# Kernel tuning notes

Hardware: AMD Instinct MI355X
Metric: run time of the kernel (lower is better)

Reference implementation:

```python
import jax, jax.numpy as jnp
import numpy as np

B, T, F = 32, 1024, 64
H = 128          # num_lstm_out
KH = 16          # kan_hidden_dim
C1, C2, C3 = 128, 256, 128
NC = 10


def _glorot(key, shape):
    fan_in = shape[0] if len(shape) == 2 else int(np.prod(shape[1:]))
    return (jax.random.normal(key, shape, jnp.float32) / np.sqrt(fan_in)).astype(jnp.float32)


def setup_inputs() -> dict:
    key = jax.random.key(0)
    ks = jax.random.split(key, 24)
    D = F + H
    d = {}
    d['x'] = jax.random.normal(ks[0], (B, T, F), jnp.float32)
    d['eps_z'] = jax.random.normal(ks[1], (B, H), jnp.float32)
    d['eps_cat'] = jax.random.normal(ks[2], (B, H), jnp.float32)
    # KAN-LSTM cell: gates = W2 @ silu(W1 @ [x;h])
    d['kan_w1'] = _glorot(ks[3], (D, KH)); d['kan_b1'] = jnp.zeros((KH,), jnp.float32)
    d['kan_w2'] = _glorot(ks[4], (KH, 4 * H)); d['kan_b2'] = jnp.zeros((4 * H,), jnp.float32)
    # causal convs (OIH layout)
    d['conv1_w'] = _glorot(ks[5], (C1, F, 8)); d['conv1_b'] = jnp.zeros((C1,), jnp.float32)
    d['conv2_w'] = _glorot(ks[6], (C2, C1, 5)); d['conv2_b'] = jnp.zeros((C2,), jnp.float32)
    d['conv3_w'] = _glorot(ks[7], (C3, C2, 3)); d['conv3_b'] = jnp.zeros((C3,), jnp.float32)
    # batchnorm affine params
    d['bn1_g'] = jnp.ones((C1,), jnp.float32); d['bn1_b'] = jnp.zeros((C1,), jnp.float32)
    d['bn2_g'] = jnp.ones((C2,), jnp.float32); d['bn2_b'] = jnp.zeros((C2,), jnp.float32)
    d['bn3_g'] = jnp.ones((C3,), jnp.float32); d['bn3_b'] = jnp.zeros((C3,), jnp.float32)
    # SE layers (reduction=16, no bias)
    d['se1_w1'] = _glorot(ks[8], (C1, C1 // 16)); d['se1_w2'] = _glorot(ks[9], (C1 // 16, C1))
    d['se2_w1'] = _glorot(ks[10], (C2, C2 // 16)); d['se2_w2'] = _glorot(ks[11], (C2 // 16, C2))
    # VIB heads
    d['fc_mu_w'] = _glorot(ks[12], (H, H)); d['fc_mu_b'] = jnp.zeros((H,), jnp.float32)
    d['fc_std_w'] = _glorot(ks[13], (H, H)); d['fc_std_b'] = jnp.zeros((H,), jnp.float32)
    d['fc_mu_cat_w'] = _glorot(ks[14], (2 * H, H)); d['fc_mu_cat_b'] = jnp.zeros((H,), jnp.float32)
    d['fc_std_cat_w'] = _glorot(ks[15], (2 * H, H)); d['fc_std_cat_b'] = jnp.zeros((H,), jnp.float32)
    d['fc_w'] = _glorot(ks[16], (H + C3, NC)); d['fc_b'] = jnp.zeros((NC,), jnp.float32)
    return d


def _kan_lstm(x, w1, b1, w2, b2):
    # x: (B,T,F) -> hidden (B,T,H); sequential recurrence via lax.scan
    xT = jnp.swapaxes(x, 0, 1)  # (T,B,F)
    h0 = jnp.zeros((x.shape[0], H), x.dtype)
    c0 = jnp.zeros((x.shape[0], H), x.dtype)

    def step(carry, xt):
        h, c = carry
        g = jax.nn.silu(jnp.concatenate([xt, h], axis=-1) @ w1 + b1) @ w2 + b2  # (B,4H)
        i_, f_, g_, o_ = jnp.split(g, 4, axis=-1)
        c = jax.nn.sigmoid(f_) * c + jax.nn.sigmoid(i_) * jnp.tanh(g_)
        h = jax.nn.sigmoid(o_) * jnp.tanh(c)
        return (h, c), h

    _, hs = jax.lax.scan(step, (h0, c0), xT)
    return jnp.swapaxes(hs, 0, 1)  # (B,T,H)


def _cluster_hidden(hidden):
    # hidden: (B,T,H). Pairwise cosine sim -> exp kernel -> best 2-block cut.
    Tn = hidden.shape[1]
    last = hidden[:, -1, :]
    hn = hidden / jnp.clip(jnp.linalg.norm(hidden, axis=-1, keepdims=True), 1e-8)
    S = jnp.exp(-5.5 * (1.0 - jnp.einsum('bik,bjk->bij', hn, hn)))  # (B,T,T)
    S = S * (1.0 - jnp.eye(Tn, dtype=S.dtype))  # zero diagonal
    # 2D prefix sums give all block sums in O(T^2) instead of O(T^3)
    P = jnp.cumsum(jnp.cumsum(S, axis=1), axis=2)
    i = jnp.arange(1, Tn)
    TL = P[:, i - 1, i - 1]                 # (B,T-1) sum of [:i,:i]
    full = P[:, -1, -1][:, None]
    TR = P[:, i - 1, -1] - TL               # sum of [:i,i:]
    BL = P[:, -1, i - 1] - TL               # sum of [i:,:i]
    BR = full - TL - TR - BL                # sum of [i:,i:]
    ii = i.astype(S.dtype)
    nn = (Tn - i).astype(S.dtype)
    dist = TL / (ii * ii) + BR / (nn * nn) - (TR + BL) / (ii * nn)
    cuts = jnp.argmax(dist, axis=1) + 1     # (B,)
    mask = (jnp.arange(Tn)[None, :] < cuts[:, None]).astype(hidden.dtype)
    corr = jnp.einsum('bt,bth->bh', mask, hidden) / cuts[:, None].astype(hidden.dtype)
    return last, corr


def _causal_conv(x, w, b):
    k = w.shape[-1]
    xp = jnp.pad(x, ((0, 0), (0, 0), (k - 1, 0)))
    y = jax.lax.conv_general_dilated(xp, w, (1,), 'VALID',
                                     dimension_numbers=('NCH', 'OIH', 'NCH'))
    return y + b[None, :, None]


def _bn(x, g, b, eps=1e-3):
    m = x.mean(axis=(0, 2), keepdims=True)
    v = x.var(axis=(0, 2), keepdims=True)
    return (x - m) / jnp.sqrt(v + eps) * g[None, :, None] + b[None, :, None]


def _se(x, w1, w2):
    y = x.mean(axis=2)                       # (B,C)
    y = jax.nn.sigmoid(jax.nn.relu(y @ w1) @ w2)
    return x * y[:, :, None]


def reference(x, eps_z, eps_cat, kan_w1, kan_b1, kan_w2, kan_b2,
              conv1_w, conv1_b, conv2_w, conv2_b, conv3_w, conv3_b,
              bn1_g, bn1_b, bn2_g, bn2_b, bn3_g, bn3_b,
              se1_w1, se1_w2, se2_w1, se2_w2,
              fc_mu_w, fc_mu_b, fc_std_w, fc_std_b,
              fc_mu_cat_w, fc_mu_cat_b, fc_std_cat_w, fc_std_cat_b,
              fc_w, fc_b):
    # LSTM branch
    hidden = _kan_lstm(x, kan_w1, kan_b1, kan_w2, kan_b2)      # (B,T,H)
    out, corr = _cluster_hidden(hidden)
    mu = corr @ fc_mu_w + fc_mu_b
    std = jax.nn.softplus(corr @ fc_std_w + fc_std_b)
    z = mu + std * eps_z
    xz = jnp.concatenate([out, z], axis=1)                      # (B,2H)
    mu_cat = xz @ fc_mu_cat_w + fc_mu_cat_b
    std_cat = jax.nn.softplus(xz @ fc_std_cat_w + fc_std_cat_b)
    x1 = mu_cat + std_cat * eps_cat   # dropout in eval mode = identity
    # FCN branch
    x2 = jnp.swapaxes(x, 1, 2)                                  # (B,F,T)
    x2 = jax.nn.gelu(_bn(_causal_conv(x2, conv1_w, conv1_b), bn1_g, bn1_b), approximate=False)
    x2 = _se(x2, se1_w1, se1_w2)
    x2 = jax.nn.gelu(_bn(_causal_conv(x2, conv2_w, conv2_b), bn2_g, bn2_b), approximate=False)
    x2 = _se(x2, se2_w1, se2_w2)
    x2 = jax.nn.gelu(_bn(_causal_conv(x2, conv3_w, conv3_b), bn3_g, bn3_b), approximate=False)
    x2 = x2.mean(axis=2)                                        # (B,C3)
    x_all = jnp.concatenate([x1, x2], axis=1)
    logits = x_all @ fc_w + fc_b
    return (jax.nn.log_softmax(logits, axis=1), mu, std, mu_cat, std_cat)
```

## Files before the change

### kernel.cpp

```cpp
#include <hip/hip_runtime.h>
#include <math.h>

#define B_ 32
#define T_ 1024
#define F_ 64
#define H_ 128
#define D_ 192
#define KH_ 16
#define C1_ 128
#define C2_ 256
#define C3_ 128
#define NC_ 10

typedef float v2f __attribute__((ext_vector_type(2)));
typedef float f32x4 __attribute__((ext_vector_type(4)));
typedef __bf16 bfrag __attribute__((ext_vector_type(8)));

__device__ __forceinline__ float sig_(float x){ return 1.f/(1.f+__expf(-x)); }
__device__ __forceinline__ float tanh_(float x){ return 1.f - 2.f/(__expf(2.f*x)+1.f); }
__device__ __forceinline__ float gelu_(float x){ return 0.5f*x*(1.f+erff(x*0.70710678118654752f)); }
__device__ __forceinline__ float softplus_(float x){ return fmaxf(x,0.f) + log1pf(__expf(-fabsf(x))); }

__device__ __forceinline__ unsigned bfpack(float a, float b){
  unsigned ua = __float_as_uint(a), ub = __float_as_uint(b);
  ua = ua + 0x7FFFu + ((ua>>16)&1u);
  ub = ub + 0x7FFFu + ((ub>>16)&1u);
  return (ua>>16) | (ub & 0xFFFF0000u);
}
__device__ __forceinline__ unsigned short bf1(float a){
  unsigned ua = __float_as_uint(a);
  ua = ua + 0x7FFFu + ((ua>>16)&1u);
  return (unsigned short)(ua>>16);
}
__device__ __forceinline__ float bf2f(unsigned short h){
  return __uint_as_float(((unsigned)h)<<16);
}

#define QPERM_XOR1(x) __int_as_float(__builtin_amdgcn_mov_dpp(__float_as_int(x), 0xB1, 0xF, 0xF, true))
#define QPERM_XOR2(x) __int_as_float(__builtin_amdgcn_mov_dpp(__float_as_int(x), 0x4E, 0xF, 0xF, true))

#define LDS_BARRIER() asm volatile("s_waitcnt lgkmcnt(0)\n\ts_barrier" ::: "memory")


__device__ __forceinline__ void ax_body(int blk, char* smemraw,
    const float* __restrict__ x, const float* __restrict__ w1, const float* __restrict__ b1,
    float* __restrict__ axT)
{
  struct AxS { float xs[16][68]; float w1s[64][16]; };
  AxS* sm = (AxS*)smemraw;
  const int bt0 = blk*16;
  const int tid = threadIdx.x;
  for(int i=tid;i<64*16;i+=256){ sm->w1s[i>>4][i&15] = w1[i]; }
  for(int i=tid;i<16*64;i+=256){ const int r=i>>6, d=i&63; sm->xs[r][d] = x[(size_t)(bt0+r)*64 + d]; }
  __syncthreads();
  const int r = tid>>4, j = tid&15;
  float s = b1[j];
  #pragma unroll
  for(int d=0; d<64; d++) s += sm->xs[r][d]*sm->w1s[d][j];
  const int bt = bt0 + r;
  axT[((size_t)(bt>>10)*16 + j)*1024 + (bt&1023)] = s;
}

__device__ __forceinline__ void prepack_body(int blk,
    const float* __restrict__ w1s, const float* __restrict__ w2s, const float* __restrict__ w3s,
    unsigned short* __restrict__ wp1, unsigned short* __restrict__ wp2, unsigned short* __restrict__ wp3)
{
  int e = blk*256 + threadIdx.x;
  if(e >= 65536+163840+98304) return;
  const float* w; unsigned short* wp; int Cout, Cin, Kw;
  if(e < 65536){ w=w1s; wp=wp1; Cout=C1_; Cin=F_;  Kw=8; }
  else if(e < 65536+163840){ e-=65536; w=w2s; wp=wp2; Cout=C2_; Cin=C1_; Kw=5; }
  else { e-=229376; w=w3s; wp=wp3; Cout=C3_; Cin=C2_; Kw=3; }
  const int co = e/(Cin*Kw);
  const int rem = e - co*(Cin*Kw);
  const int ci = rem/Kw, kw = rem - ci*Kw;
  const int off = (((ci>>5)*Kw + kw)*(Cout>>4) + (co>>4))*512 + ((co&15)*4 + ((ci>>3)&3))*8 + (ci&7);
  wp[off] = bf1(w[e]);
}

__device__ __forceinline__ void norm_body(int blk,
    const float* __restrict__ hidden,
    unsigned short* __restrict__ hnhi, unsigned short* __restrict__ hnlo)
{
  const int row = blk*8 + (threadIdx.x>>5);
  const int l = threadIdx.x&31;
  const float* hr = hidden + (size_t)row*H_;
  float s = 0.f;
  for(int k=l;k<H_;k+=32){ float v=hr[k]; s+=v*v; }
  #pragma unroll
  for(int m=16;m>=1;m>>=1) s += __shfl_xor(s, m, 64);
  const float inv = 1.f/fmaxf(sqrtf(s), 1e-8f);
  const float4 v = *(const float4*)&hr[l*4];
  const float f0=v.x*inv, f1=v.y*inv, f2=v.z*inv, f3=v.w*inv;
  const unsigned short h0=bf1(f0), h1=bf1(f1), h2=bf1(f2), h3=bf1(f3);
  uint2 phi; phi.x = (unsigned)h0 | ((unsigned)h1<<16); phi.y = (unsigned)h2 | ((unsigned)h3<<16);
  *(uint2*)&hnhi[(size_t)row*H_ + l*4] = phi;
  const unsigned short g0=bf1(f0-bf2f(h0)), g1=bf1(f1-bf2f(h1)), g2=bf1(f2-bf2f(h2)), g3=bf1(f3-bf2f(h3));
  uint2 plo; plo.x = (unsigned)g0 | ((unsigned)g1<<16); plo.y = (unsigned)g2 | ((unsigned)g3<<16);
  *(uint2*)&hnlo[(size_t)row*H_ + l*4] = plo;
}

struct SS {
  unsigned short Ahi[64*136];
  unsigned short Alo[64*136];
  unsigned short Bhi[64*136];
  unsigned short Blo[64*136];
  double red[64][17];
};
__device__ __forceinline__ void s_body(int blk, char* smemraw,
    const unsigned short* __restrict__ hnhi, const unsigned short* __restrict__ hnlo,
    double* __restrict__ rowsum, double* __restrict__ psum)
{
  SS* sm = (SS*)smemraw;
  const int b = blk >> 4;
  const int i0 = (blk & 15) * 64;
  const int tid = threadIdx.x, l = tid & 63, wv = tid >> 6;
  const int m = l & 15, q = l >> 4;

  {
    const uint4* ghi = (const uint4*)(hnhi + ((size_t)b*T_ + i0)*H_);
    const uint4* glo = (const uint4*)(hnlo + ((size_t)b*T_ + i0)*H_);
    for(int idx=tid; idx<64*16; idx+=256){
      const int r = idx>>4, c8 = idx&15;
      *(uint4*)&sm->Ahi[r*136 + c8*8] = ghi[r*16 + c8];
      *(uint4*)&sm->Alo[r*136 + c8*8] = glo[r*16 + c8];
    }
  }

  double rs[4]={0,0,0,0}, ps[4]={0,0,0,0};
  const int arow = (wv*16 + m)*136;

  for(int jt=0;jt<16;jt++){
    const int j0 = jt*64;
    __syncthreads();
    {
      const uint4* ghi = (const uint4*)(hnhi + ((size_t)b*T_ + j0)*H_);
      const uint4* glo = (const uint4*)(hnlo + ((size_t)b*T_ + j0)*H_);
      for(int idx=tid; idx<64*16; idx+=256){
        const int r = idx>>4, c8 = idx&15;
        *(uint4*)&sm->Bhi[r*136 + c8*8] = ghi[r*16 + c8];
        *(uint4*)&sm->Blo[r*136 + c8*8] = glo[r*16 + c8];
      }
    }
    __syncthreads();

    f32x4 acc[4];
    #pragma unroll
    for(int nt=0;nt<4;nt++) acc[nt] = (f32x4)(0.f);
    #pragma unroll
    for(int kc=0;kc<4;kc++){
      const bfrag Ah = *(const bfrag*)&sm->Ahi[arow + kc*32 + q*8];
      const bfrag Al = *(const bfrag*)&sm->Alo[arow + kc*32 + q*8];
      #pragma unroll
      for(int nt=0;nt<4;nt++){
        const int brow = (nt*16 + m)*136 + kc*32 + q*8;
        const bfrag Bh = *(const bfrag*)&sm->Bhi[brow];
        const bfrag Bl = *(const bfrag*)&sm->Blo[brow];
        acc[nt] = __builtin_amdgcn_mfma_f32_16x16x32_bf16(Ah, Bh, acc[nt], 0, 0, 0);
        acc[nt] = __builtin_amdgcn_mfma_f32_16x16x32_bf16(Al, Bh, acc[nt], 0, 0, 0);
        acc[nt] = __builtin_amdgcn_mfma_f32_16x16x32_bf16(Ah, Bl, acc[nt], 0, 0, 0);
      }
    }
    #pragma unroll
    for(int nt=0;nt<4;nt++){
      const int gj = j0 + nt*16 + m;
      #pragma unroll
      for(int r=0;r<4;r++){
        const int gi = i0 + wv*16 + q*4 + r;
        if(gi == gj) continue;
        const float sv = __expf(-5.5f*(1.f - acc[nt][r]));
        rs[r] += (double)sv;
        if(gj < gi) ps[r] += (double)sv;
      }
    }
  }
  __syncthreads();
  #pragma unroll
  for(int r=0;r<4;r++) sm->red[wv*16 + q*4 + r][m] = rs[r];
  __syncthreads();
  if(tid<64){ double v=0; for(int k=0;k<16;k++) v+=sm->red[tid][k]; rowsum[(size_t)b*T_ + i0 + tid]=v; }
  __syncthreads();
  #pragma unroll
  for(int r=0;r<4;r++) sm->red[wv*16 + q*4 + r][m] = ps[r];
  __syncthreads();
  if(tid<64){ double v=0; for(int k=0;k<16;k++) v+=sm->red[tid][k]; psum[(size_t)b*T_ + i0 + tid]=v; }
}

struct CS {
  double sr[256]; double sp[256]; double bd[256]; double totR;
  float c2[2][128]; int bidx[256]; int cut;
};
__device__ __forceinline__ void cluster_body(int b, char* smemraw,
    const double* __restrict__ rowsum, const double* __restrict__ psum,
    const float* __restrict__ hidden, float* __restrict__ corr, int* __restrict__ cuts)
{
  CS* sm = (CS*)smemraw;
  const int tid = threadIdx.x;
  const double* r = rowsum + (size_t)b*T_;
  const double* p = psum + (size_t)b*T_;
  double r4[4], p4[4];
  #pragma unroll
  for(int q=0;q<4;q++){ r4[q]=r[tid*4+q]; p4[q]=p[tid*4+q]; }
  sm->sr[tid]=r4[0]+r4[1]+r4[2]+r4[3];
  sm->sp[tid]=p4[0]+p4[1]+p4[2]+p4[3];
  __syncthreads();
  if(tid==0){
    double ar=0, ap=0;
    for(int i=0;i<256;i++){ double tr=sm->sr[i], tp=sm->sp[i]; sm->sr[i]=ar; sm->sp[i]=ap; ar+=tr; ap+=tp; }
    sm->totR = ar;
  }
  __syncthreads();
  double cr = sm->sr[tid], cp = sm->sp[tid];
  const double full = sm->totR;
  double best = -1e308; int bi = 1;
  #pragma unroll
  for(int q=0;q<4;q++){
    cr += r4[q]; cp += p4[q];
    const int i = 4*tid + q + 1;
    if(i < T_){
      const double TL = 2.0*cp;
      const double TRv = cr - TL;
      const double BR = full - TL - 2.0*TRv;
      const double di = (double)i, dn = (double)(T_-i);
      const double dist = TL/(di*di) + BR/(dn*dn) - (2.0*TRv)/(di*dn);
      if(dist > best){ best=dist; bi=i; }
    }
  }
  sm->bd[tid]=best; sm->bidx[tid]=bi;
  __syncthreads();
  if(tid==0){
    double bb=-1e308; int ii=1;
    for(int q=0;q<256;q++){ if(sm->bd[q]>bb){ bb=sm->bd[q]; ii=sm->bidx[q]; } }
    sm->cut=ii; cuts[b]=ii;
  }
  __syncthreads();
  const int cut = sm->cut;
  const int h = tid&127, half = tid>>7;
  float s=0.f;
  const float* hb = hidden + (size_t)b*T_*H_;
  #pragma unroll 4
  for(int t=half; t<cut; t+=2) s += hb[(size_t)t*H_ + h];
  sm->c2[half][h]=s;
  __syncthreads();
  if(tid<128) corr[b*H_+tid] = (sm->c2[0][tid]+sm->c2[1][tid])/(float)cut;
}

__device__ __forceinline__ void head1_body(int b, char* smemraw,
    const float* __restrict__ corr, const float* __restrict__ hidden,
    const float* __restrict__ eps_z, const float* __restrict__ eps_cat,
    const float* __restrict__ mu_w, const float* __restrict__ mu_b,
    const float* __restrict__ std_w, const float* __restrict__ std_b,
    const float* __restrict__ muc_w, const float* __restrict__ muc_b,
    const float* __restrict__ stdc_w, const float* __restrict__ stdc_b,
    float* __restrict__ out_mu, float* __restrict__ out_std,
    float* __restrict__ out_muc, float* __restrict__ out_stdc, float* __restrict__ x1)
{
  struct H1 { float cs[128]; float xz[256]; };
  H1* sm = (H1*)smemraw;
  const int h = threadIdx.x;
  if(h<128){
    sm->cs[h]=corr[b*H_+h];
    sm->xz[h]=hidden[((size_t)b*T_ + (T_-1))*H_ + h];
  }
  __syncthreads();
  if(h<128){
    float m=mu_b[h], sdv=std_b[h];
    for(int k=0;k<H_;k++){ const float cv=sm->cs[k]; m+=cv*mu_w[k*H_+h]; sdv+=cv*std_w[k*H_+h]; }
    const float stdv = softplus_(sdv);
    out_mu[b*H_+h]=m; out_std[b*H_+h]=stdv;
    sm->xz[128+h] = m + stdv*eps_z[b*H_+h];
  }
  __syncthreads();
  if(h<128){
    float mc=muc_b[h], sc=stdc_b[h];
    for(int k=0;k<256;k++){ const float v=sm->xz[k]; mc+=v*muc_w[k*H_+h]; sc+=v*stdc_w[k*H_+h]; }
    const float stdc = softplus_(sc);
    out_muc[b*H_+h]=mc; out_stdc[b*H_+h]=stdc;
    x1[b*H_+h]=mc + stdc*eps_cat[b*H_+h];
  }
}

struct ConvS {
  float sescale[256];
  float seh[16];
  unsigned short xs[72*40];
};
__device__ __forceinline__ void conv_body(int bx, int by, int bz, char* smemraw,
    const float* __restrict__ in, const unsigned short* __restrict__ wp,
    const float* __restrict__ bias,
    const float* __restrict__ se_in, const float* __restrict__ se_w1,
    const float* __restrict__ se_w2, int seR,
    float* __restrict__ y, float* __restrict__ bnacc, int Cin, int Cout, int Kw)
{
  ConvS* sm = (ConvS*)smemraw;
  unsigned short* xs = sm->xs;
  const int b = bz, t0 = bx*64, co0 = by*64;
  const int tid = threadIdx.x, l = tid&63, wv = tid>>6;
  const int q = l>>4, m = l&15;
  const int TW = 64 + Kw - 1;
  const int abase = (wv*16 + m)*40 + q*8;
  const int boff = (m*4 + q)*8;
  const bool use_se = (se_in != nullptr);

  if(use_se){
    float* ms = (float*)xs;
    if(tid<Cin) ms[tid] = se_in[b*Cin+tid] * (1.f/(float)T_);
    __syncthreads();
    if(tid<seR){ float s=0.f; for(int k=0;k<Cin;k++) s += ms[k]*se_w1[k*seR+tid]; sm->seh[tid]=fmaxf(s,0.f); }
    __syncthreads();
    if(tid<Cin){ float s=0.f; for(int k=0;k<seR;k++) s += sm->seh[k]*se_w2[k*Cin+tid]; sm->sescale[tid]=sig_(s); }
  }

  f32x4 acc[4];
  #pragma unroll
  for(int nt=0;nt<4;nt++) acc[nt] = (f32x4)(0.f);

  const int nchunks = Cin >> 5;
  for(int cc=0; cc<nchunks; cc++){
    __syncthreads();
    for(int idx=tid; idx<TW*8; idx+=256){
      const int r = idx>>3, c4 = (idx&7)*4;
      const int tg = t0 - (Kw-1) + r;
      uint2 pk = make_uint2(0u, 0u);
      if(tg >= 0){
        float4 v = *(const float4*)&in[((size_t)b*T_ + tg)*Cin + cc*32 + c4];
        if(use_se){
          const float4 s4 = *(const float4*)&sm->sescale[cc*32 + c4];
          v.x*=s4.x; v.y*=s4.y; v.z*=s4.z; v.w*=s4.w;
        }
        pk.x = bfpack(v.x, v.y); pk.y = bfpack(v.z, v.w);
      }
      *(uint2*)&xs[r*40 + c4] = pk;
    }
    __syncthreads();
    for(int kw=0; kw<Kw; kw++){
      const bfrag Af = *(const bfrag*)&xs[abase + kw*40];
      #pragma unroll
      for(int nt=0; nt<4; nt++){
        const unsigned short* wpp = wp + ((size_t)((cc*Kw + kw)*(Cout>>4) + (by*4 + nt)))*512 + boff;
        const bfrag Bf = *(const bfrag*)wpp;
        acc[nt] = __builtin_amdgcn_mfma_f32_16x16x32_bf16(Af, Bf, acc[nt], 0, 0, 0);
      }
    }
  }
  __syncthreads();
  float* part = (float*)xs;
  const int t_base = t0 + wv*16 + q*4;
  #pragma unroll
  for(int nt=0; nt<4; nt++){
    const int co = co0 + nt*16 + m;
    const float bv = bias[co];
    float s1 = 0.f, s2 = 0.f;
    #pragma unroll
    for(int r=0;r<4;r++){
      const float v = acc[nt][r] + bv;
      y[((size_t)b*T_ + t_base + r)*Cout + co] = v;
      s1 += v; s2 += v*v;
    }
    s1 += __shfl_xor(s1, 16); s1 += __shfl_xor(s1, 32);
    s2 += __shfl_xor(s2, 16); s2 += __shfl_xor(s2, 32);
    if(q==0){ part[(wv*64 + nt*16 + m)*2+0] = s1; part[(wv*64 + nt*16 + m)*2+1] = s2; }
  }
  __syncthreads();
  if(tid < 64){
    float a1=0.f, a2=0.f;
    #pragma unroll
    for(int w2i=0; w2i<4; w2i++){ a1 += part[(w2i*64+tid)*2+0]; a2 += part[(w2i*64+tid)*2+1]; }
    atomicAdd(&bnacc[co0 + tid], a1);
    atomicAdd(&bnacc[Cout + co0 + tid], a2);
  }
}

__device__ __forceinline__ void bn_act_body(int b, int chunk, char* smemraw,
    float* __restrict__ y, const float* __restrict__ bnacc,
    const float* __restrict__ gw, const float* __restrict__ bw,
    float* __restrict__ mean_acc, int C, int write_y)
{
  const int t0 = chunk*128, tid = threadIdx.x;
  const int c = tid & (C-1), part = tid / C, np = 256 / C;
  const float cnt = (float)(B_*T_);
  const float mm = bnacc[c]/cnt;
  const float var = bnacc[C+c]/cnt - mm*mm;
  const float sc = gw[c]/sqrtf(var+1e-3f);
  const float sh = bw[c] - mm*sc;
  float s = 0.f;
  for(int t=t0+part; t<t0+128; t+=np){
    const size_t off = ((size_t)b*T_ + t)*C + c;
    float v = y[off];
    v = gelu_(v*sc + sh);
    if(write_y) y[off] = v;
    s += v;
  }
  float* rs = (float*)smemraw;
  if(np > 1){
    rs[tid]=s;
    __syncthreads();
    if(part==0) s += rs[tid+C];
  }
  if(part==0) atomicAdd(&mean_acc[b*C+c], s);
}

__device__ __forceinline__ void se_body(int b, char* smemraw,
    const float* __restrict__ mean_in, const float* __restrict__ w1, const float* __restrict__ w2,
    float* __restrict__ scale, int C, int R)
{
  struct SE { float ms[256]; float hs2[16]; };
  SE* sm = (SE*)smemraw;
  const int tid=threadIdx.x;
  if(tid<C) sm->ms[tid]=mean_in[b*C+tid]*(1.f/(float)T_);
  __syncthreads();
  if(tid<R){ float s=0; for(int k=0;k<C;k++) s+=sm->ms[k]*w1[k*R+tid]; sm->hs2[tid]=fmaxf(s,0.f); }
  __syncthreads();
  if(tid<C){ float s=0; for(int k=0;k<R;k++) s+=sm->hs2[k]*w2[k*C+tid]; scale[b*C+tid]=sig_(s); }
}


__global__ __launch_bounds__(256) void mega0_kernel(
    const float* c1w, const float* c2w, const float* c3w,
    unsigned short* wp1, unsigned short* wp2, unsigned short* wp3,
    const float* x, const float* kw1, const float* kb1, float* axT)
{
  __shared__ __align__(16) char sm[16*68*4 + 64*16*4];
  const int bid = blockIdx.x;
  if(bid < 1280) prepack_body(bid, c1w, c2w, c3w, wp1, wp2, wp3);
  else ax_body(bid-1280, sm, x, kw1, kb1, axT);
}

__global__ __launch_bounds__(128, 1) void lstm_kernel(
    const float* __restrict__ axT, const float* __restrict__ w1,
    const float* __restrict__ w2, const float* __restrict__ b2,
    float* __restrict__ hidden)
{
  __shared__ float hs[2][148];
  const int b = blockIdx.x, tid = threadIdx.x;
  const int l = tid & 63, wv = tid >> 6;
  const int j = l >> 2, g = l & 3;
  const int hi = wv*64 + l;

  v2f w1hv[16];
  #pragma unroll
  for(int q=0;q<16;q++){
    w1hv[q].x = w1[(64 + g*32 + 2*q)*KH_ + j];
    w1hv[q].y = w1[(64 + g*32 + 2*q + 1)*KH_ + j];
  }
  v2f w2if[16], w2go[16];
  #pragma unroll
  for(int k=0;k<16;k++){
    w2if[k].x = w2[k*512 + hi];       w2if[k].y = w2[k*512 + 128 + hi];
    w2go[k].x = w2[k*512 + 256 + hi]; w2go[k].y = w2[k*512 + 384 + hi];
  }
  v2f bif, bgo;
  bif.x = b2[hi]; bif.y = b2[128+hi]; bgo.x = b2[256+hi]; bgo.y = b2[384+hi];

  for(int i=tid;i<2*148;i+=128) ((float*)hs)[i]=0.f;
  float c = 0.f;
  const float* axr = axT + ((size_t)b*16 + j)*1024;
  float* hb = hidden + (size_t)b*T_*H_;
  const int hwi = (hi>>5)*36 + (hi&31);
  float4 axA = *(const float4*)&axr[0];
  float4 axB = *(const float4*)&axr[4];
  __syncthreads();

#define LSTM_STEP(tt, axv, RB) { \
    const float* hsr = hs[RB]; \
    float* hsw = hs[1-(RB)]; \
    v2f ap0=(v2f)(0.f), ap1=(v2f)(0.f), ap2=(v2f)(0.f), ap3=(v2f)(0.f); \
    { const float4 hv = *(const float4*)&hsr[g*36 + 0];  ap0 += ((v2f){hv.x,hv.y})*w1hv[0]  + ((v2f){hv.z,hv.w})*w1hv[1]; } \
    { const float4 hv = *(const float4*)&hsr[g*36 + 4];  ap1 += ((v2f){hv.x,hv.y})*w1hv[2]  + ((v2f){hv.z,hv.w})*w1hv[3]; } \
    { const float4 hv = *(const float4*)&hsr[g*36 + 8];  ap2 += ((v2f){hv.x,hv.y})*w1hv[4]  + ((v2f){hv.z,hv.w})*w1hv[5]; } \
    { const float4 hv = *(const float4*)&hsr[g*36 + 12]; ap3 += ((v2f){hv.x,hv.y})*w1hv[6]  + ((v2f){hv.z,hv.w})*w1hv[7]; } \
    { const float4 hv = *(const float4*)&hsr[g*36 + 16]; ap0 += ((v2f){hv.x,hv.y})*w1hv[8]  + ((v2f){hv.z,hv.w})*w1hv[9]; } \
    { const float4 hv = *(const float4*)&hsr[g*36 + 20]; ap1 += ((v2f){hv.x,hv.y})*w1hv[10] + ((v2f){hv.z,hv.w})*w1hv[11]; } \
    { const float4 hv = *(const float4*)&hsr[g*36 + 24]; ap2 += ((v2f){hv.x,hv.y})*w1hv[12] + ((v2f){hv.z,hv.w})*w1hv[13]; } \
    { const float4 hv = *(const float4*)&hsr[g*36 + 28]; ap3 += ((v2f){hv.x,hv.y})*w1hv[14] + ((v2f){hv.z,hv.w})*w1hv[15]; } \
    const v2f apt = (ap0+ap1)+(ap2+ap3); \
    float a = apt.x + apt.y; \
    a += QPERM_XOR1(a); \
    a += QPERM_XOR2(a); \
    a += (axv); \
    const float g1 = a * sig_(a); \
    v2f aIF = bif, aGO = bgo; \
    _Pragma("unroll") \
    for(int k=0;k<16;k++){ \
      const float gk = __int_as_float(__builtin_amdgcn_readlane(__float_as_int(g1), 4*k)); \
      v2f gk2; gk2.x=gk; gk2.y=gk; \
      aIF += gk2 * w2if[k]; \
      aGO += gk2 * w2go[k]; \
    } \
    const float si = sig_(aIF.x); \
    const float sf = sig_(aIF.y); \
    const float tg = tanh_(aGO.x); \
    const float so = sig_(aGO.y); \
    c = sf*c + si*tg; \
    const float h = so * tanh_(c); \
    hsw[hwi] = h; \
    hb[(size_t)(tt)*H_ + hi] = h; \
    LDS_BARRIER(); \
  }

  for(int t0=0;t0<T_;t0+=4){
    const int tl = (t0+8 < 1020) ? (t0+8) : 1020;
    const float4 axC = *(const float4*)&axr[tl];
    LSTM_STEP(t0+0, axA.x, 0)
    LSTM_STEP(t0+1, axA.y, 1)
    LSTM_STEP(t0+2, axA.z, 0)
    LSTM_STEP(t0+3, axA.w, 1)
    axA = axB; axB = axC;
  }
#undef LSTM_STEP
}

__global__ __launch_bounds__(256) void megaA_kernel(
    const float* x, const unsigned short* wp1, const float* c1b, float* y1, float* bn1,
    const float* hidden, unsigned short* hnhi, unsigned short* hnlo)
{
  __shared__ __align__(16) char sm[sizeof(ConvS)];
  const int bid = blockIdx.x;
  if(bid < 1024) conv_body(bid&15, (bid>>4)&1, bid>>5, sm, x, wp1, c1b,
                           nullptr, nullptr, nullptr, 0, y1, bn1, F_, C1_, 8);
  else norm_body(bid-1024, hidden, hnhi, hnlo);
}

__global__ __launch_bounds__(256) void megaB_kernel(
    const unsigned short* hnhi, const unsigned short* hnlo, double* rowsum, double* psum,
    float* y1, const float* bn1, const float* g1w, const float* b1w, float* se1_in)
{
  __shared__ __align__(16) char sm[sizeof(SS)];
  const int bid = blockIdx.x;
  if(bid < 512) s_body(bid, sm, hnhi, hnlo, rowsum, psum);
  else { const int cb = bid-512; bn_act_body(cb>>3, cb&7, sm, y1, bn1, g1w, b1w, se1_in, C1_, 1); }
}

__global__ __launch_bounds__(256) void megaC_kernel(
    const double* rowsum, const double* psum, const float* hidden, float* corr, int* cuts,
    const float* y1, const unsigned short* wp2, const float* c2b,
    const float* se1_in, const float* s1w1, const float* s1w2,
    float* y2, float* bn2)
{
  __shared__ __align__(16) char sm[sizeof(CS) > sizeof(ConvS) ? sizeof(CS) : sizeof(ConvS)];
  const int bid = blockIdx.x;
  if(bid < 32) cluster_body(bid, sm, rowsum, psum, hidden, corr, cuts);
  else {
    const int cb = bid - 32;
    conv_body(cb&15, (cb>>4)&3, cb>>6, sm, y1, wp2, c2b,
              se1_in, s1w1, s1w2, C1_/16, y2, bn2, C1_, C2_, 5);
  }
}

__global__ __launch_bounds__(256) void megaD_kernel(
    const float* corr, const float* hidden, const float* eps_z, const float* eps_cat,
    const float* mu_w, const float* mu_b, const float* std_w, const float* std_b,
    const float* muc_w, const float* muc_b, const float* stdc_w, const float* stdc_b,
    float* out_mu, float* out_std, float* out_muc, float* out_stdc, float* x1,
    float* y2, const float* bn2, const float* g2w, const float* b2w, float* se2_in)
{
  __shared__ __align__(16) char sm[1536];
  const int bid = blockIdx.x;
  if(bid < 32) head1_body(bid, sm, corr, hidden, eps_z, eps_cat, mu_w, mu_b, std_w, std_b,
                          muc_w, muc_b, stdc_w, stdc_b, out_mu, out_std, out_muc, out_stdc, x1);
  else { const int cb = bid-32; bn_act_body(cb>>3, cb&7, sm, y2, bn2, g2w, b2w, se2_in, C2_, 1); }
}

__global__ __launch_bounds__(256) void conv3_kernel(
    const float* y2, const unsigned short* wp3, const float* c3b,
    const float* se2_in, const float* s2w1, const float* s2w2,
    float* y3, float* bn3)
{
  __shared__ __align__(16) char sm[sizeof(ConvS)];
  const int bid = blockIdx.x;
  conv_body(bid&15, (bid>>4)&1, bid>>5, sm, y2, wp3, c3b,
            se2_in, s2w1, s2w2, C2_/16, y3, bn3, C2_, C3_, 3);
}

__global__ __launch_bounds__(256) void bn3_kernel(
    float* y3, const float* bn3, const float* g3w, const float* b3w, float* x2)
{
  __shared__ __align__(16) char sm[1024];
  const int bid = blockIdx.x;
  bn_act_body(bid>>3, bid&7, sm, y3, bn3, g3w, b3w, x2, C3_, 0);
}

__global__ __launch_bounds__(64) void head2_kernel(
    const float* __restrict__ x1, const float* __restrict__ x2,
    const float* __restrict__ fcw, const float* __restrict__ fcb, float* __restrict__ outls)
{
  const int b=blockIdx.x, tid=threadIdx.x;
  __shared__ float xa[256]; __shared__ float lg[NC_];
  for(int k=tid;k<256;k+=64) xa[k] = (k<128)? x1[b*128+k] : x2[b*128+(k-128)]*(1.f/(float)T_);
  __syncthreads();
  if(tid<NC_){
    float s = fcb[tid];
    for(int k=0;k<256;k++) s += xa[k]*fcw[k*NC_+tid];
    lg[tid]=s;
  }
  __syncthreads();
  if(tid==0){
    float mx=lg[0];
    for(int q=1;q<NC_;q++) mx=fmaxf(mx,lg[q]);
    float se=0;
    for(int q=0;q<NC_;q++) se += __expf(lg[q]-mx);
    const float lse = logf(se)+mx;
    for(int q=0;q<NC_;q++) outls[b*NC_+q] = lg[q]-lse;
  }
}

extern "C" void kernel_launch(void* const* d_in, const int* in_sizes, int n_in,
                              void* d_out, int out_size, void* d_ws, size_t ws_size,
                              hipStream_t stream) {
  (void)in_sizes; (void)n_in; (void)out_size; (void)ws_size;
  const float* x        = (const float*)d_in[0];
  const float* eps_z    = (const float*)d_in[1];
  const float* eps_cat  = (const float*)d_in[2];
  const float* kan_w1   = (const float*)d_in[3];
  const float* kan_b1   = (const float*)d_in[4];
  const float* kan_w2   = (const float*)d_in[5];
  const float* kan_b2   = (const float*)d_in[6];
  const float* conv1_w  = (const float*)d_in[7];
  const float* conv1_b  = (const float*)d_in[8];
  const float* conv2_w  = (const float*)d_in[9];
  const float* conv2_b  = (const float*)d_in[10];
  const float* conv3_w  = (const float*)d_in[11];
  const float* conv3_b  = (const float*)d_in[12];
  const float* bn1_g    = (const float*)d_in[13];
  const float* bn1_b    = (const float*)d_in[14];
  const float* bn2_g    = (const float*)d_in[15];
  const float* bn2_b    = (const float*)d_in[16];
  const float* bn3_g    = (const float*)d_in[17];
  const float* bn3_b    = (const float*)d_in[18];
  const float* se1_w1   = (const float*)d_in[19];
  const float* se1_w2   = (const float*)d_in[20];
  const float* se2_w1   = (const float*)d_in[21];
  const float* se2_w2   = (const float*)d_in[22];
  const float* fc_mu_w  = (const float*)d_in[23];
  const float* fc_mu_b  = (const float*)d_in[24];
  const float* fc_std_w = (const float*)d_in[25];
  const float* fc_std_b = (const float*)d_in[26];
  const float* fc_muc_w = (const float*)d_in[27];
  const float* fc_muc_b = (const float*)d_in[28];
  const float* fc_stdc_w= (const float*)d_in[29];
  const float* fc_stdc_b= (const float*)d_in[30];
  const float* fc_w     = (const float*)d_in[31];
  const float* fc_b     = (const float*)d_in[32];

  float* out = (float*)d_out;
  float* out_ls   = out;
  float* out_mu   = out + 320;
  float* out_std  = out + 320 + 4096;
  float* out_muc  = out + 320 + 2*4096;
  float* out_stdc = out + 320 + 3*4096;

  float* ws = (float*)d_ws;
  const size_t SZ_HID = (size_t)B_*T_*H_;
  const size_t SZ_Y1  = (size_t)B_*T_*C1_;
  const size_t SZ_Y2  = (size_t)B_*T_*C2_;
  float*  hidden = ws;
  float*  y1     = hidden + SZ_HID;
  float*  y2     = y1 + SZ_Y1;
  double* rowsum = (double*)(y2 + SZ_Y2);
  double* psum   = rowsum + (size_t)B_*T_;
  float*  corr   = (float*)(psum + (size_t)B_*T_);
  float*  x1     = corr + (size_t)B_*H_;
  float*  bnbuf  = x1 + (size_t)B_*H_;
  float*  bn1    = bnbuf;
  float*  bn2    = bnbuf + 2*C1_;
  float*  bn3    = bnbuf + 2*C1_ + 2*C2_;
  float*  se1_in = bnbuf + 1024;
  float*  se2_in = se1_in + (size_t)B_*C1_;
  float*  x2     = se2_in + (size_t)B_*C2_;
  int*    cuts   = (int*)(x2 + (size_t)B_*C3_);
  float*  axbuf  = (float*)(cuts + B_);
  unsigned short* wp1 = (unsigned short*)(axbuf + (size_t)B_*16*T_);
  unsigned short* wp2 = wp1 + (size_t)C1_*F_*8;
  unsigned short* wp3 = wp2 + (size_t)C2_*C1_*5;
  unsigned short* hnhi = wp3 + (size_t)C3_*C2_*3;
  unsigned short* hnlo = hnhi + (size_t)B_*T_*H_;
  float*  y3     = y1;

  hipMemsetAsync(bnbuf, 0, (size_t)(1024 + B_*C1_ + B_*C2_ + B_*C3_)*sizeof(float), stream);

  mega0_kernel<<<3328, 256, 0, stream>>>(conv1_w, conv2_w, conv3_w, wp1, wp2, wp3,
                                         x, kan_w1, kan_b1, axbuf);
  lstm_kernel<<<B_, 128, 0, stream>>>(axbuf, kan_w1, kan_w2, kan_b2, hidden);
  megaA_kernel<<<1024 + 4096, 256, 0, stream>>>(x, wp1, conv1_b, y1, bn1, hidden, hnhi, hnlo);
  megaB_kernel<<<512 + 256, 256, 0, stream>>>(hnhi, hnlo, rowsum, psum,
                                              y1, bn1, bn1_g, bn1_b, se1_in);
  megaC_kernel<<<32 + 2048, 256, 0, stream>>>(rowsum, psum, hidden, corr, cuts,
                                              y1, wp2, conv2_b, se1_in, se1_w1, se1_w2, y2, bn2);
  megaD_kernel<<<32 + 256, 256, 0, stream>>>(corr, hidden, eps_z, eps_cat,
      fc_mu_w, fc_mu_b, fc_std_w, fc_std_b, fc_muc_w, fc_muc_b, fc_stdc_w, fc_stdc_b,
      out_mu, out_std, out_muc, out_stdc, x1,
      y2, bn2, bn2_g, bn2_b, se2_in);
  conv3_kernel<<<1024, 256, 0, stream>>>(y2, wp3, conv3_b, se2_in, se2_w1, se2_w2, y3, bn3);
  bn3_kernel<<<256, 256, 0, stream>>>(y3, bn3, bn3_g, bn3_b, x2);
  head2_kernel<<<B_, 64, 0, stream>>>(x1, x2, fc_w, fc_b, out_ls);
}
```

Measured before the change: 900.8 us.

## Split LSTM gate math across lane pairs using 256 threads per block

Doubles the LSTM block from 128 to 256 threads so each hidden unit is handled by a lane pair. One lane computes the input and forget gates and the other the cell-candidate and output gates, each doing half the second-layer matvec and exchanging results via a quad permute. This shortens the per-step serial critical path of the recurrence. In exchange the first-layer reduction is done redundantly by 4 waves, and the cell update is duplicated in both lanes. The unused se_body helper is removed.

```diff
diff --git a/kernel.cpp b/kernel.cpp
--- a/kernel.cpp
+++ b/kernel.cpp
@@ -400,20 +400,6 @@
   if(part==0) atomicAdd(&mean_acc[b*C+c], s);
 }
 
-__device__ __forceinline__ void se_body(int b, char* smemraw,
-    const float* __restrict__ mean_in, const float* __restrict__ w1, const float* __restrict__ w2,
-    float* __restrict__ scale, int C, int R)
-{
-  struct SE { float ms[256]; float hs2[16]; };
-  SE* sm = (SE*)smemraw;
-  const int tid=threadIdx.x;
-  if(tid<C) sm->ms[tid]=mean_in[b*C+tid]*(1.f/(float)T_);
-  __syncthreads();
-  if(tid<R){ float s=0; for(int k=0;k<C;k++) s+=sm->ms[k]*w1[k*R+tid]; sm->hs2[tid]=fmaxf(s,0.f); }
-  __syncthreads();
-  if(tid<C){ float s=0; for(int k=0;k<R;k++) s+=sm->hs2[k]*w2[k*C+tid]; scale[b*C+tid]=sig_(s); }
-}
-
 
 __global__ __launch_bounds__(256) void mega0_kernel(
     const float* c1w, const float* c2w, const float* c3w,
@@ -426,16 +412,17 @@
   else ax_body(bid-1280, sm, x, kw1, kb1, axT);
 }
 
-__global__ __launch_bounds__(128, 1) void lstm_kernel(
+__global__ __launch_bounds__(256, 1) void lstm_kernel(
     const float* __restrict__ axT, const float* __restrict__ w1,
     const float* __restrict__ w2, const float* __restrict__ b2,
     float* __restrict__ hidden)
 {
   __shared__ float hs[2][148];
   const int b = blockIdx.x, tid = threadIdx.x;
-  const int l = tid & 63, wv = tid >> 6;
+  const int l = tid & 63;
   const int j = l >> 2, g = l & 3;
-  const int hi = wv*64 + l;
+  const int p = tid & 1;
+  const int hi = tid >> 1;
 
   v2f w1hv[16];
   #pragma unroll
@@ -443,16 +430,16 @@
     w1hv[q].x = w1[(64 + g*32 + 2*q)*KH_ + j];
     w1hv[q].y = w1[(64 + g*32 + 2*q + 1)*KH_ + j];
   }
-  v2f w2if[16], w2go[16];
+  const int go = p ? 256 : 0;
+  v2f w2r[16];
   #pragma unroll
   for(int k=0;k<16;k++){
-    w2if[k].x = w2[k*512 + hi];       w2if[k].y = w2[k*512 + 128 + hi];
-    w2go[k].x = w2[k*512 + 256 + hi]; w2go[k].y = w2[k*512 + 384 + hi];
-  }
-  v2f bif, bgo;
-  bif.x = b2[hi]; bif.y = b2[128+hi]; bgo.x = b2[256+hi]; bgo.y = b2[384+hi];
-
-  for(int i=tid;i<2*148;i+=128) ((float*)hs)[i]=0.f;
+    w2r[k].x = w2[k*512 + go + hi];
+    w2r[k].y = w2[k*512 + go + 128 + hi];
+  }
+  v2f bp; bp.x = b2[go + hi]; bp.y = b2[go + 128 + hi];
+
+  for(int i=tid;i<2*148;i+=256) ((float*)hs)[i]=0.f;
   float c = 0.f;
   const float* axr = axT + ((size_t)b*16 + j)*1024;
   float* hb = hidden + (size_t)b*T_*H_;
@@ -478,23 +465,25 @@
     a += QPERM_XOR1(a); \
     a += QPERM_XOR2(a); \
     a += (axv); \
-    const float g1 = a * sig_(a); \
-    v2f aIF = bif, aGO = bgo; \
+    const float g1v = a * sig_(a); \
+    v2f aP = bp; \
     _Pragma("unroll") \
     for(int k=0;k<16;k++){ \
-      const float gk = __int_as_float(__builtin_amdgcn_readlane(__float_as_int(g1), 4*k)); \
+      const float gk = __int_as_float(__builtin_amdgcn_readlane(__float_as_int(g1v), 4*k)); \
       v2f gk2; gk2.x=gk; gk2.y=gk; \
-      aIF += gk2 * w2if[k]; \
-      aGO += gk2 * w2go[k]; \
+      aP += gk2 * w2r[k]; \
     } \
-    const float si = sig_(aIF.x); \
-    const float sf = sig_(aIF.y); \
-    const float tg = tanh_(aGO.x); \
-    const float so = sig_(aGO.y); \
-    c = sf*c + si*tg; \
-    const float h = so * tanh_(c); \
-    hsw[hwi] = h; \
-    hb[(size_t)(tt)*H_ + hi] = h; \
+    const float A0 = aP.x, A1 = aP.y; \
+    const float arg0 = p ? (A0+A0) : A0; \
+    const float s0 = sig_(arg0); \
+    const float v0 = p ? (s0+s0-1.f) : s0;    \
+    const float v1 = sig_(A1);                \
+    const float tgx = QPERM_XOR1(v0);         \
+    const float sox = QPERM_XOR1(v1);         \
+    c = v1*c + v0*tgx; \
+    const float t2 = tanh_(c); \
+    const float h = sox * t2; \
+    if(!p){ hsw[hwi] = h; hb[(size_t)(tt)*H_ + hi] = h; } \
     LDS_BARRIER(); \
   }
 
@@ -680,7 +669,7 @@
 
   mega0_kernel<<<3328, 256, 0, stream>>>(conv1_w, conv2_w, conv3_w, wp1, wp2, wp3,
                                          x, kan_w1, kan_b1, axbuf);
-  lstm_kernel<<<B_, 128, 0, stream>>>(axbuf, kan_w1, kan_w2, kan_b2, hidden);
+  lstm_kernel<<<B_, 256, 0, stream>>>(axbuf, kan_w1, kan_w2, kan_b2, hidden);
   megaA_kernel<<<1024 + 4096, 256, 0, stream>>>(x, wp1, conv1_b, y1, bn1, hidden, hnhi, hnlo);
   megaB_kernel<<<512 + 256, 256, 0, stream>>>(hnhi, hnlo, rowsum, psum,
                                               y1, bn1, bn1_g, bn1_b, se1_in);
```

Measured after the change: 958.7 us. 6.4% more time.
